# Kernel tuning notes

Hardware: AMD Instinct MI355X
Metric: run time of the kernel (lower is better)

## Reference

```python
import jax, jax.numpy as jnp
import numpy as np

NUM_NODES = 100000
NUM_EDGES = 1600000
DIM = 64
TAU = 0.5
EPS = 1e-12
SURGERY_EPS = 1e-6


def setup_inputs() -> dict:
    key = jax.random.key(0)
    k1, k2, k3, k4, k5 = jax.random.split(key, 5)
    x = jax.random.normal(k1, (NUM_NODES, DIM), dtype=jnp.float32)
    edge_index = jax.random.randint(k2, (2, NUM_EDGES), 0, NUM_NODES, dtype=jnp.int64)
    edge_weight = jax.random.uniform(k3, (NUM_EDGES,), dtype=jnp.float32)
    # nn.Linear weights (no bias): y = x @ W.T
    W_self = jax.random.normal(k4, (DIM, DIM), dtype=jnp.float32) / np.sqrt(DIM)
    W_neigh = jax.random.normal(k5, (DIM, DIM), dtype=jnp.float32) / np.sqrt(DIM)
    return {"x": x, "edge_index": edge_index, "edge_weight": edge_weight,
            "W_self": W_self, "W_neigh": W_neigh}


def reference(x, edge_index, edge_weight, W_self, W_neigh):
    num_nodes = x.shape[0]
    row, col = edge_index[0], edge_index[1]

    # --- Ollivier-Ricci (LLY limit-free combinatorial lower-bound) curvature per edge ---
    deg = jax.ops.segment_sum(edge_weight, row, num_segments=num_nodes)  # weighted out-degree
    inv_du = 1.0 / jnp.maximum(deg[row], EPS)
    inv_dv = 1.0 / jnp.maximum(deg[col], EPS)
    kappa = 2.0 * inv_du + 2.0 * inv_dv - 2.0  # [E]

    # --- CFL-stable step size for the Ricci flow ---
    delta_t = 0.5 / (jnp.max(jnp.abs(kappa)) + 1e-6)

    # --- Ricci-flow half step: dw/dt = -kappa * w ---
    w_half = jnp.maximum(edge_weight * (1.0 - 0.5 * delta_t * kappa), 0.0)

    # --- metric surgery: drop degenerate edges (implemented as a zero-weight mask,
    #     keeping edge count static so the kernel is jit-compatible) ---
    mask = w_half > SURGERY_EPS
    w_half = jnp.where(mask, w_half, 0.0)

    # --- row normalisation ---
    row_sum = jax.ops.segment_sum(w_half, row, num_segments=num_nodes)
    w_norm = w_half / jnp.maximum(row_sum[row], EPS)

    # --- Laplacian off-diagonals: L_uv = -w_norm  =>  -L_uv = w_norm ---
    minus_L = w_norm

    # --- incident mean curvature per node (over surviving edges) -> curvature gate ---
    cnt = jax.ops.segment_sum(mask.astype(x.dtype), row, num_segments=num_nodes)
    k_sum = jax.ops.segment_sum(jnp.where(mask, kappa, 0.0), row, num_segments=num_nodes)
    mean_kappa = k_sum / jnp.maximum(cnt, 1.0)
    rho = jax.nn.sigmoid(mean_kappa)  # [N]

    # --- gated message passing ---
    h_self = x @ W_self.T    # [N, D]
    h_neigh = x @ W_neigh.T  # [N, D]
    msg = minus_L[:, None] * h_neigh[col]                      # [E, D] gather + scale
    neigh_aggr = jax.ops.segment_sum(msg, row, num_segments=num_nodes)  # scatter-add

    # h0 buffer == first-forward x (detached)
    out = rho[:, None] * h_self + neigh_aggr + TAU * x
    return out, edge_index, w_norm
```

## Files before the change

### kernel.cpp

```cpp
#include <hip/hip_runtime.h>
#include <math.h>

#define NNODES 100000
#define NEDGES 1600000
#define DIM 64
#define TAU 0.5f
#define EPSF 1e-12f
#define SEPS 1e-6f

#define K 256
#define RPB 391
#define TILE 4096
#define EPT 8
#define CAP 7168
#define MAXK_GRID 512

typedef unsigned long long ull;
typedef unsigned short u16;
typedef __attribute__((ext_vector_type(8))) short bf16x8;
typedef __attribute__((ext_vector_type(4))) float f32x4;

__device__ __forceinline__ float bf2f(u16 h) {
    return __uint_as_float((unsigned)h << 16);
}
__device__ __forceinline__ u16 f2bf(float f) {
    unsigned u = __float_as_uint(f);
    u += 0x7FFFu + ((u >> 16) & 1);
    return (u16)(u >> 16);
}

__global__ __launch_bounds__(256) void k_init(int* __restrict__ bcur,
                                              float* __restrict__ maxabs) {
    bcur[threadIdx.x] = threadIdx.x * CAP;
    if (threadIdx.x < 4) maxabs[threadIdx.x] = 0.0f;
}

__global__ __launch_bounds__(512) void k_bin(const int* __restrict__ ei, const float* __restrict__ w,
                                             int* __restrict__ bcur, ull* __restrict__ arena,
                                             int E, int N) {
    __shared__ ull stg[TILE];
    __shared__ unsigned char bkt[TILE];
    __shared__ int cnt[K], lscan[K], gbase[K], cur[K], sc[K];
    __shared__ int tot;
    int t = threadIdx.x;
    int e0 = blockIdx.x * TILE;
    if (t < K) { cnt[t] = 0; cur[t] = 0; }
    __syncthreads();
    ull rec[EPT];
    int bb[EPT];
#pragma unroll
    for (int j = 0; j < EPT; j++) {
        int e = e0 + t + j * 512;
        bb[j] = -1;
        if (e < E) {
            int r = min(max(ei[e], 0), N - 1);
            int c = min(max(ei[E + e], 0), N - 1);
            float wv = w[e];
            int b = r / RPB, lr = r - b * RPB;
            rec[j] = ((ull)__float_as_uint(wv) << 32) | (unsigned)(c | (lr << 17));
            bb[j] = b;
            atomicAdd(&cnt[b], 1);
        }
    }
    __syncthreads();
    int v = (t < K) ? cnt[t] : 0;
    if (t < K) sc[t] = v;
    __syncthreads();
    for (int o = 1; o < K; o <<= 1) {
        int a = (t >= o && t < K) ? sc[t - o] : 0;
        __syncthreads();
        if (t < K) sc[t] += a;
        __syncthreads();
    }
    if (t < K) {
        lscan[t] = sc[t] - v;
        if (v > 0) gbase[t] = atomicAdd(&bcur[t], v);
        if (t == K - 1) tot = sc[t];
    }
    __syncthreads();
#pragma unroll
    for (int j = 0; j < EPT; j++) {
        if (bb[j] >= 0) {
            int p = lscan[bb[j]] + atomicAdd(&cur[bb[j]], 1);
            stg[p] = rec[j];
            bkt[p] = (unsigned char)bb[j];
        }
    }
    __syncthreads();
    int T = tot;
    for (int i = t; i < T; i += 512) {
        int b = bkt[i];
        size_t pos = (size_t)gbase[b] + (i - lscan[b]);
        if (pos < (size_t)(b + 1) * CAP) arena[pos] = stg[i];
    }
}

__global__ __launch_bounds__(512) void k_sort(const int* __restrict__ bcur,
                                              ull* __restrict__ arena,
                                              float* __restrict__ invdeg,
                                              int* __restrict__ off, int* __restrict__ degi,
                                              int N) {
    __shared__ ull stg[CAP];
    __shared__ int hist[RPB];
    __shared__ float degl[RPB];
    __shared__ int cur[RPB];
    __shared__ int sc[512];
    int t = threadIdx.x, b = blockIdx.x;
    int base = b * CAP;
    int cnt = min(bcur[b] - base, CAP);
    for (int i = t; i < RPB; i += 512) { hist[i] = 0; degl[i] = 0.0f; cur[i] = 0; }
    __syncthreads();
    for (int i = t; i < cnt; i += 512) {
        ull rec = arena[base + i];
        stg[i] = rec;
        int lr = (int)((rec >> 17) & 0x1FF);
        atomicAdd(&hist[lr], 1);
        atomicAdd(&degl[lr], __uint_as_float((unsigned)(rec >> 32)));
    }
    __syncthreads();
    int v = (t < RPB) ? hist[t] : 0;
    sc[t] = v;
    __syncthreads();
    for (int o = 1; o < 512; o <<= 1) {
        int a = (t >= o) ? sc[t - o] : 0;
        __syncthreads();
        sc[t] += a;
        __syncthreads();
    }
    int ex = sc[t] - v;
    if (t < RPB) {
        hist[t] = ex;
        int rn = b * RPB + t;
        if (rn < N) {
            off[rn] = base + ex; degi[rn] = v;
            invdeg[rn] = 1.0f / fmaxf(degl[t], EPSF);
        }
    }
    __syncthreads();
    int2* out2 = (int2*)arena;
    for (int i = t; i < cnt; i += 512) {
        ull rec = stg[i];
        int lr = (int)((rec >> 17) & 0x1FF);
        int p = hist[lr] + atomicAdd(&cur[lr], 1);
        out2[base + p] = make_int2((int)(rec & 0x1FFFF), (int)(unsigned)(rec >> 32));
    }
}

__global__ __launch_bounds__(256) void k_maxk(const int* __restrict__ ei,
                                              const float* __restrict__ invdeg,
                                              float* __restrict__ maxabs, int E, int N) {
    float m = 0.0f;
    int stride = gridDim.x * 256;
    for (int e = blockIdx.x * 256 + threadIdx.x; e < E; e += stride) {
        int r = min(max(ei[e], 0), N - 1);
        int c = min(max(ei[E + e], 0), N - 1);
        m = fmaxf(m, fabsf(2.0f * invdeg[r] + 2.0f * invdeg[c] - 2.0f));
    }
    for (int o = 32; o > 0; o >>= 1) m = fmaxf(m, __shfl_down(m, o, 64));
    __shared__ float red[4];
    int lane = threadIdx.x & 63, wid = threadIdx.x >> 6;
    if (lane == 0) red[wid] = m;
    __syncthreads();
    if (threadIdx.x == 0) {
        float bm = fmaxf(fmaxf(red[0], red[1]), fmaxf(red[2], red[3]));
        atomicMax((unsigned int*)maxabs, __float_as_uint(bm));
    }
}

#define WL(mp, d, kk) (((mp) * 64 + (d)) * 72 + (kk))
__global__ __launch_bounds__(256) void k_gemm(const float* __restrict__ x,
                                              const float* __restrict__ Wself,
                                              const float* __restrict__ Wneigh,
                                              u16* __restrict__ hneigh_h,
                                              float* __restrict__ out, int N) {
    __shared__ u16 wlds[4 * 64 * 72];
    int t = threadIdx.x;
    for (int i = t; i < 4096; i += 256) {
        int d = i >> 6, k = i & 63;
        float v = Wself[i];
        u16 h = f2bf(v);
        u16 lo = f2bf(v - bf2f(h));
        wlds[WL(0, d, k)] = h;
        wlds[WL(1, d, k)] = lo;
        v = Wneigh[i];
        h = f2bf(v);
        lo = f2bf(v - bf2f(h));
        wlds[WL(2, d, k)] = h;
        wlds[WL(3, d, k)] = lo;
    }
    __syncthreads();
    int w = t >> 6, l = t & 63;
    int m = l & 15, kg = l >> 4;
    int n0 = blockIdx.x * 64 + w * 16;
    if (n0 >= N) return;
    int nodeA = n0 + m;
    bf16x8 ah[2], al[2];
#pragma unroll
    for (int ks = 0; ks < 2; ks++) {
        float v[8];
        if (nodeA < N) {
            const float4* xp = (const float4*)(x + (size_t)nodeA * 64 + ks * 32 + kg * 8);
            float4 v0 = xp[0], v1 = xp[1];
            v[0] = v0.x; v[1] = v0.y; v[2] = v0.z; v[3] = v0.w;
            v[4] = v1.x; v[5] = v1.y; v[6] = v1.z; v[7] = v1.w;
        } else {
#pragma unroll
            for (int j = 0; j < 8; j++) v[j] = 0.0f;
        }
#pragma unroll
        for (int j = 0; j < 8; j++) {
            u16 h = f2bf(v[j]);
            u16 lo = f2bf(v[j] - bf2f(h));
            ah[ks][j] = (short)h;
            al[ks][j] = (short)lo;
        }
    }
    f32x4 accS[4], accN[4];
#pragma unroll
    for (int dt = 0; dt < 4; dt++) {
        accS[dt] = (f32x4){0.0f, 0.0f, 0.0f, 0.0f};
        accN[dt] = (f32x4){0.0f, 0.0f, 0.0f, 0.0f};
    }
#pragma unroll
    for (int dt = 0; dt < 4; dt++) {
        int d = dt * 16 + m;
#pragma unroll
        for (int ks = 0; ks < 2; ks++) {
            int kof = ks * 32 + kg * 8;
            bf16x8 bsh = *(const bf16x8*)&wlds[WL(0, d, kof)];
            bf16x8 bsl = *(const bf16x8*)&wlds[WL(1, d, kof)];
            bf16x8 bnh = *(const bf16x8*)&wlds[WL(2, d, kof)];
            bf16x8 bnl = *(const bf16x8*)&wlds[WL(3, d, kof)];
            accS[dt] = __builtin_amdgcn_mfma_f32_16x16x32_bf16(ah[ks], bsh, accS[dt], 0, 0, 0);
            accS[dt] = __builtin_amdgcn_mfma_f32_16x16x32_bf16(al[ks], bsh, accS[dt], 0, 0, 0);
            accS[dt] = __builtin_amdgcn_mfma_f32_16x16x32_bf16(ah[ks], bsl, accS[dt], 0, 0, 0);
            accN[dt] = __builtin_amdgcn_mfma_f32_16x16x32_bf16(ah[ks], bnh, accN[dt], 0, 0, 0);
            accN[dt] = __builtin_amdgcn_mfma_f32_16x16x32_bf16(al[ks], bnh, accN[dt], 0, 0, 0);
            accN[dt] = __builtin_amdgcn_mfma_f32_16x16x32_bf16(ah[ks], bnl, accN[dt], 0, 0, 0);
        }
    }
    int rbase = kg * 4;
#pragma unroll
    for (int r = 0; r < 4; r++) {
        int nn = n0 + rbase + r;
        if (nn >= N) continue;
#pragma unroll
        for (int dt = 0; dt < 4; dt++) {
            int d = dt * 16 + m;
            size_t idx = (size_t)nn * 64 + d;
            out[idx] = accS[dt][r];
            hneigh_h[idx] = f2bf(accN[dt][r]);
        }
    }
}

__global__ __launch_bounds__(256) void k_aggr(const int* __restrict__ off,
                                              const int* __restrict__ degi,
                                              const float* __restrict__ invdeg,
                                              const int2* __restrict__ csr,
                                              const float* __restrict__ maxabs,
                                              const float* __restrict__ x,
                                              const u16* __restrict__ hneigh_h,
                                              float* __restrict__ row_sum,
                                              float* __restrict__ out, int N) {
    int t = threadIdx.x;
    int lane = t & 63;
    int q = lane & 15;
    int g = lane >> 4;
    int n = blockIdx.x * 4 + (t >> 6);
    if (n >= N) return;
    int s = off[n], end = s + degi[n];
    float dt = 0.5f / (*maxabs + 1e-6f);
    float c1 = -0.5f * dt;
    float a = 2.0f * invdeg[n] - 2.0f;
    const ushort4* hn4 = (const ushort4*)hneigh_h;
    float a0 = 0.0f, a1 = 0.0f, a2 = 0.0f, a3 = 0.0f;
    float rs = 0.0f, ks = 0.0f, ct = 0.0f;
    int i = s;
    for (; i + 16 <= end; i += 16) {
        int2 p0 = csr[i + g];
        int2 p1 = csr[i + 4 + g];
        int2 p2 = csr[i + 8 + g];
        int2 p3 = csr[i + 12 + g];
        ushort4 h0 = hn4[(unsigned)((p0.x << 4) | q)];
        ushort4 h1 = hn4[(unsigned)((p1.x << 4) | q)];
        ushort4 h2 = hn4[(unsigned)((p2.x << 4) | q)];
        ushort4 h3 = hn4[(unsigned)((p3.x << 4) | q)];
        float k0 = fmaf(2.0f, invdeg[p0.x], a), k1 = fmaf(2.0f, invdeg[p1.x], a);
        float k2 = fmaf(2.0f, invdeg[p2.x], a), k3 = fmaf(2.0f, invdeg[p3.x], a);
        float w0 = __int_as_float(p0.y) * fmaf(c1, k0, 1.0f);
        float w1 = __int_as_float(p1.y) * fmaf(c1, k1, 1.0f);
        float w2 = __int_as_float(p2.y) * fmaf(c1, k2, 1.0f);
        float w3 = __int_as_float(p3.y) * fmaf(c1, k3, 1.0f);
        bool m0 = w0 > SEPS, m1 = w1 > SEPS, m2 = w2 > SEPS, m3 = w3 > SEPS;
        w0 = m0 ? w0 : 0.0f;
        w1 = m1 ? w1 : 0.0f;
        w2 = m2 ? w2 : 0.0f;
        w3 = m3 ? w3 : 0.0f;
        rs += (w0 + w1) + (w2 + w3);
        ks += ((m0 ? k0 : 0.0f) + (m1 ? k1 : 0.0f)) + ((m2 ? k2 : 0.0f) + (m3 ? k3 : 0.0f));
        ct += ((m0 ? 1.0f : 0.0f) + (m1 ? 1.0f : 0.0f)) + ((m2 ? 1.0f : 0.0f) + (m3 ? 1.0f : 0.0f));
        a0 = fmaf(w0, bf2f(h0.x), a0); a1 = fmaf(w0, bf2f(h0.y), a1);
        a2 = fmaf(w0, bf2f(h0.z), a2); a3 = fmaf(w0, bf2f(h0.w), a3);
        a0 = fmaf(w1, bf2f(h1.x), a0); a1 = fmaf(w1, bf2f(h1.y), a1);
        a2 = fmaf(w1, bf2f(h1.z), a2); a3 = fmaf(w1, bf2f(h1.w), a3);
        a0 = fmaf(w2, bf2f(h2.x), a0); a1 = fmaf(w2, bf2f(h2.y), a1);
        a2 = fmaf(w2, bf2f(h2.z), a2); a3 = fmaf(w2, bf2f(h2.w), a3);
        a0 = fmaf(w3, bf2f(h3.x), a0); a1 = fmaf(w3, bf2f(h3.y), a1);
        a2 = fmaf(w3, bf2f(h3.z), a2); a3 = fmaf(w3, bf2f(h3.w), a3);
    }
    for (; i < end; i += 4) {
        int e = i + g;
        bool v = e < end;
        int2 p = make_int2(0, 0);
        if (v) p = csr[e];
        ushort4 h = hn4[(unsigned)((p.x << 4) | q)];
        float kk = fmaf(2.0f, invdeg[p.x], a);
        float wv = __int_as_float(p.y) * fmaf(c1, kk, 1.0f);
        bool m = v && (wv > SEPS);
        wv = m ? wv : 0.0f;
        rs += wv;
        ks += m ? kk : 0.0f;
        ct += m ? 1.0f : 0.0f;
        a0 = fmaf(wv, bf2f(h.x), a0);
        a1 = fmaf(wv, bf2f(h.y), a1);
        a2 = fmaf(wv, bf2f(h.z), a2);
        a3 = fmaf(wv, bf2f(h.w), a3);
    }
    a0 += __shfl_xor(a0, 16, 64);
    a1 += __shfl_xor(a1, 16, 64);
    a2 += __shfl_xor(a2, 16, 64);
    a3 += __shfl_xor(a3, 16, 64);
    rs += __shfl_xor(rs, 16, 64);
    ks += __shfl_xor(ks, 16, 64);
    ct += __shfl_xor(ct, 16, 64);
    a0 += __shfl_xor(a0, 32, 64);
    a1 += __shfl_xor(a1, 32, 64);
    a2 += __shfl_xor(a2, 32, 64);
    a3 += __shfl_xor(a3, 32, 64);
    rs += __shfl_xor(rs, 32, 64);
    ks += __shfl_xor(ks, 32, 64);
    ct += __shfl_xor(ct, 32, 64);
    float mk = ks / fmaxf(ct, 1.0f);
    float rho = 1.0f / (1.0f + expf(-mk));
    float inv_rs = 1.0f / fmaxf(rs, EPSF);
    if (g == 0) {
        float4* o4 = (float4*)(out + (size_t)n * 64);
        const float4* x4 = (const float4*)(x + (size_t)n * 64);
        float4 o = o4[q];
        float4 xv = x4[q];
        o.x = fmaf(rho, o.x, fmaf(TAU, xv.x, a0 * inv_rs));
        o.y = fmaf(rho, o.y, fmaf(TAU, xv.y, a1 * inv_rs));
        o.z = fmaf(rho, o.z, fmaf(TAU, xv.z, a2 * inv_rs));
        o.w = fmaf(rho, o.w, fmaf(TAU, xv.w, a3 * inv_rs));
        o4[q] = o;
        if (q == 0) row_sum[n] = rs;
    }
}

__global__ void k_final(const int* __restrict__ ei, const float* __restrict__ w,
                        const float* __restrict__ invdeg, const float* __restrict__ row_sum,
                        const float* __restrict__ maxabs,
                        float* __restrict__ out_ei, float* __restrict__ out_wn, int E, int N) {
    int e = blockIdx.x * blockDim.x + threadIdx.x;
    if (e >= E) return;
    int r0 = ei[e], c0 = ei[E + e];
    int r = min(max(r0, 0), N - 1);
    int c = min(max(c0, 0), N - 1);
    float dt = 0.5f / (*maxabs + 1e-6f);
    float kap = 2.0f * invdeg[r] + 2.0f * invdeg[c] - 2.0f;
    float wh = fmaxf(w[e] * (1.0f - 0.5f * dt * kap), 0.0f);
    if (wh <= SEPS) wh = 0.0f;
    out_wn[e] = wh / fmaxf(row_sum[r], EPSF);
    out_ei[e] = (float)r0;
    out_ei[E + e] = (float)c0;
}

extern "C" void kernel_launch(void* const* d_in, const int* in_sizes, int n_in,
                              void* d_out, int out_size, void* d_ws, size_t ws_size,
                              hipStream_t stream) {
    (void)in_sizes; (void)n_in; (void)out_size; (void)ws_size;
    const int N = NNODES, E = NEDGES;

    const float* x      = (const float*)d_in[0];
    const int*   ei     = (const int*)d_in[1];
    const float* w      = (const float*)d_in[2];
    const float* Wself  = (const float*)d_in[3];
    const float* Wneigh = (const float*)d_in[4];

    float* out    = (float*)d_out;
    float* out_ei = out + (size_t)N * DIM;
    float* out_wn = out_ei + 2 * (size_t)E;

    ull*  arena = (ull*)out_ei;
    int2* csr   = (int2*)out_ei;

    float* invdeg  = (float*)d_ws;
    int*   off     = (int*)d_ws + (size_t)N;
    int*   degi    = (int*)d_ws + 2 * (size_t)N;
    float* row_sum = (float*)d_ws + 3 * (size_t)N;
    float* maxabs  = row_sum + (size_t)N;
    int*   bcur    = (int*)(maxabs + 4);
    u16*   hneigh_h = (u16*)((float*)d_ws + 4 * (size_t)N + 288);

    k_init<<<1, 256, 0, stream>>>(bcur, maxabs);
    k_bin<<<(E + TILE - 1) / TILE, 512, 0, stream>>>(ei, w, bcur, arena, E, N);
    k_sort<<<K, 512, 0, stream>>>(bcur, arena, invdeg, off, degi, N);
    k_maxk<<<MAXK_GRID, 256, 0, stream>>>(ei, invdeg, maxabs, E, N);
    k_gemm<<<(N + 63) / 64, 256, 0, stream>>>(x, Wself, Wneigh, hneigh_h, out, N);
    k_aggr<<<(N + 3) / 4, 256, 0, stream>>>(off, degi, invdeg, csr, maxabs, x,
                                            hneigh_h, row_sum, out, N);
    k_final<<<(E + 255) / 256, 256, 0, stream>>>(ei, w, invdeg, row_sum, maxabs,
                                                 out_ei, out_wn, E, N);
}
```

Baseline: 243.1 us.

## Fuse per-bucket sort and dense GEMM into one heterogeneous launch

```diff
diff --git a/kernel.cpp b/kernel.cpp
--- a/kernel.cpp
+++ b/kernel.cpp
@@ -14,6 +14,7 @@
 #define EPT 8
 #define CAP 7168
 #define MAXK_GRID 512
+#define GEMM_BLKS ((NNODES + 127) / 128)
 
 typedef unsigned long long ull;
 typedef unsigned short u16;
@@ -95,54 +96,149 @@
     }
 }
 
-__global__ __launch_bounds__(512) void k_sort(const int* __restrict__ bcur,
-                                              ull* __restrict__ arena,
-                                              float* __restrict__ invdeg,
-                                              int* __restrict__ off, int* __restrict__ degi,
-                                              int N) {
-    __shared__ ull stg[CAP];
-    __shared__ int hist[RPB];
-    __shared__ float degl[RPB];
-    __shared__ int cur[RPB];
-    __shared__ int sc[512];
-    int t = threadIdx.x, b = blockIdx.x;
-    int base = b * CAP;
-    int cnt = min(bcur[b] - base, CAP);
-    for (int i = t; i < RPB; i += 512) { hist[i] = 0; degl[i] = 0.0f; cur[i] = 0; }
-    __syncthreads();
-    for (int i = t; i < cnt; i += 512) {
-        ull rec = arena[base + i];
-        stg[i] = rec;
-        int lr = (int)((rec >> 17) & 0x1FF);
-        atomicAdd(&hist[lr], 1);
-        atomicAdd(&degl[lr], __uint_as_float((unsigned)(rec >> 32)));
-    }
-    __syncthreads();
-    int v = (t < RPB) ? hist[t] : 0;
-    sc[t] = v;
-    __syncthreads();
-    for (int o = 1; o < 512; o <<= 1) {
-        int a = (t >= o) ? sc[t - o] : 0;
-        __syncthreads();
-        sc[t] += a;
-        __syncthreads();
-    }
-    int ex = sc[t] - v;
-    if (t < RPB) {
-        hist[t] = ex;
-        int rn = b * RPB + t;
-        if (rn < N) {
-            off[rn] = base + ex; degi[rn] = v;
-            invdeg[rn] = 1.0f / fmaxf(degl[t], EPSF);
-        }
-    }
-    __syncthreads();
-    int2* out2 = (int2*)arena;
-    for (int i = t; i < cnt; i += 512) {
-        ull rec = stg[i];
-        int lr = (int)((rec >> 17) & 0x1FF);
-        int p = hist[lr] + atomicAdd(&cur[lr], 1);
-        out2[base + p] = make_int2((int)(rec & 0x1FFFF), (int)(unsigned)(rec >> 32));
+struct SortSmem {
+    ull stg[CAP];
+    int hist[RPB];
+    float degl[RPB];
+    int cur[RPB];
+    int sc[512];
+};
+struct GemmSmem {
+    u16 wlds[4 * 64 * 72];
+};
+#define WL(mp, d, kk) (((mp) * 64 + (d)) * 72 + (kk))
+
+__global__ __launch_bounds__(512) void k_sg(const int* __restrict__ bcur,
+                                            ull* __restrict__ arena,
+                                            float* __restrict__ invdeg,
+                                            int* __restrict__ off, int* __restrict__ degi,
+                                            const float* __restrict__ x,
+                                            const float* __restrict__ Wself,
+                                            const float* __restrict__ Wneigh,
+                                            u16* __restrict__ hneigh_h,
+                                            float* __restrict__ out, int N) {
+    __shared__ __align__(16) char smraw[sizeof(SortSmem)];
+    int t = threadIdx.x;
+    if (blockIdx.x < K) {
+        SortSmem* sm = (SortSmem*)smraw;
+        int b = blockIdx.x;
+        int base = b * CAP;
+        int cnt = min(bcur[b] - base, CAP);
+        for (int i = t; i < RPB; i += 512) { sm->hist[i] = 0; sm->degl[i] = 0.0f; sm->cur[i] = 0; }
+        __syncthreads();
+        for (int i = t; i < cnt; i += 512) {
+            ull rec = arena[base + i];
+            sm->stg[i] = rec;
+            int lr = (int)((rec >> 17) & 0x1FF);
+            atomicAdd(&sm->hist[lr], 1);
+            atomicAdd(&sm->degl[lr], __uint_as_float((unsigned)(rec >> 32)));
+        }
+        __syncthreads();
+        int v = (t < RPB) ? sm->hist[t] : 0;
+        sm->sc[t] = v;
+        __syncthreads();
+        for (int o = 1; o < 512; o <<= 1) {
+            int a = (t >= o) ? sm->sc[t - o] : 0;
+            __syncthreads();
+            sm->sc[t] += a;
+            __syncthreads();
+        }
+        int ex = sm->sc[t] - v;
+        if (t < RPB) {
+            sm->hist[t] = ex;
+            int rn = b * RPB + t;
+            if (rn < N) {
+                off[rn] = base + ex; degi[rn] = v;
+                invdeg[rn] = 1.0f / fmaxf(sm->degl[t], EPSF);
+            }
+        }
+        __syncthreads();
+        int2* out2 = (int2*)arena;
+        for (int i = t; i < cnt; i += 512) {
+            ull rec = sm->stg[i];
+            int lr = (int)((rec >> 17) & 0x1FF);
+            int p = sm->hist[lr] + atomicAdd(&sm->cur[lr], 1);
+            out2[base + p] = make_int2((int)(rec & 0x1FFFF), (int)(unsigned)(rec >> 32));
+        }
+    } else {
+        GemmSmem* sm = (GemmSmem*)smraw;
+        for (int i = t; i < 4096; i += 512) {
+            int d = i >> 6, k = i & 63;
+            float v = Wself[i];
+            u16 h = f2bf(v);
+            u16 lo = f2bf(v - bf2f(h));
+            sm->wlds[WL(0, d, k)] = h;
+            sm->wlds[WL(1, d, k)] = lo;
+            v = Wneigh[i];
+            h = f2bf(v);
+            lo = f2bf(v - bf2f(h));
+            sm->wlds[WL(2, d, k)] = h;
+            sm->wlds[WL(3, d, k)] = lo;
+        }
+        __syncthreads();
+        int w = t >> 6, l = t & 63;
+        int m = l & 15, kg = l >> 4;
+        int n0 = (blockIdx.x - K) * 128 + w * 16;
+        if (n0 >= N) return;
+        int nodeA = n0 + m;
+        bf16x8 ah[2], al[2];
+#pragma unroll
+        for (int ks = 0; ks < 2; ks++) {
+            float v[8];
+            if (nodeA < N) {
+                const float4* xp = (const float4*)(x + (size_t)nodeA * 64 + ks * 32 + kg * 8);
+                float4 v0 = xp[0], v1 = xp[1];
+                v[0] = v0.x; v[1] = v0.y; v[2] = v0.z; v[3] = v0.w;
+                v[4] = v1.x; v[5] = v1.y; v[6] = v1.z; v[7] = v1.w;
+            } else {
+#pragma unroll
+                for (int j = 0; j < 8; j++) v[j] = 0.0f;
+            }
+#pragma unroll
+            for (int j = 0; j < 8; j++) {
+                u16 h = f2bf(v[j]);
+                u16 lo = f2bf(v[j] - bf2f(h));
+                ah[ks][j] = (short)h;
+                al[ks][j] = (short)lo;
+            }
+        }
+        f32x4 accS[4], accN[4];
+#pragma unroll
+        for (int dt = 0; dt < 4; dt++) {
+            accS[dt] = (f32x4){0.0f, 0.0f, 0.0f, 0.0f};
+            accN[dt] = (f32x4){0.0f, 0.0f, 0.0f, 0.0f};
+        }
+#pragma unroll
+        for (int dt = 0; dt < 4; dt++) {
+            int d = dt * 16 + m;
+#pragma unroll
+            for (int ks = 0; ks < 2; ks++) {
+                int kof = ks * 32 + kg * 8;
+                bf16x8 bsh = *(const bf16x8*)&sm->wlds[WL(0, d, kof)];
+                bf16x8 bsl = *(const bf16x8*)&sm->wlds[WL(1, d, kof)];
+                bf16x8 bnh = *(const bf16x8*)&sm->wlds[WL(2, d, kof)];
+                bf16x8 bnl = *(const bf16x8*)&sm->wlds[WL(3, d, kof)];
+                accS[dt] = __builtin_amdgcn_mfma_f32_16x16x32_bf16(ah[ks], bsh, accS[dt], 0, 0, 0);
+                accS[dt] = __builtin_amdgcn_mfma_f32_16x16x32_bf16(al[ks], bsh, accS[dt], 0, 0, 0);
+                accS[dt] = __builtin_amdgcn_mfma_f32_16x16x32_bf16(ah[ks], bsl, accS[dt], 0, 0, 0);
+                accN[dt] = __builtin_amdgcn_mfma_f32_16x16x32_bf16(ah[ks], bnh, accN[dt], 0, 0, 0);
+                accN[dt] = __builtin_amdgcn_mfma_f32_16x16x32_bf16(al[ks], bnh, accN[dt], 0, 0, 0);
+                accN[dt] = __builtin_amdgcn_mfma_f32_16x16x32_bf16(ah[ks], bnl, accN[dt], 0, 0, 0);
+            }
+        }
+        int rbase = kg * 4;
+#pragma unroll
+        for (int r = 0; r < 4; r++) {
+            int nn = n0 + rbase + r;
+            if (nn >= N) continue;
+#pragma unroll
+            for (int dt = 0; dt < 4; dt++) {
+                int d = dt * 16 + m;
+                size_t idx = (size_t)nn * 64 + d;
+                out[idx] = accS[dt][r];
+                hneigh_h[idx] = f2bf(accN[dt][r]);
+            }
+        }
     }
 }
 
@@ -164,93 +260,6 @@
     if (threadIdx.x == 0) {
         float bm = fmaxf(fmaxf(red[0], red[1]), fmaxf(red[2], red[3]));
         atomicMax((unsigned int*)maxabs, __float_as_uint(bm));
-    }
-}
-
-#define WL(mp, d, kk) (((mp) * 64 + (d)) * 72 + (kk))
-__global__ __launch_bounds__(256) void k_gemm(const float* __restrict__ x,
-                                              const float* __restrict__ Wself,
-                                              const float* __restrict__ Wneigh,
-                                              u16* __restrict__ hneigh_h,
-                                              float* __restrict__ out, int N) {
-    __shared__ u16 wlds[4 * 64 * 72];
-    int t = threadIdx.x;
-    for (int i = t; i < 4096; i += 256) {
-        int d = i >> 6, k = i & 63;
-        float v = Wself[i];
-        u16 h = f2bf(v);
-        u16 lo = f2bf(v - bf2f(h));
-        wlds[WL(0, d, k)] = h;
-        wlds[WL(1, d, k)] = lo;
-        v = Wneigh[i];
-        h = f2bf(v);
-        lo = f2bf(v - bf2f(h));
-        wlds[WL(2, d, k)] = h;
-        wlds[WL(3, d, k)] = lo;
-    }
-    __syncthreads();
-    int w = t >> 6, l = t & 63;
-    int m = l & 15, kg = l >> 4;
-    int n0 = blockIdx.x * 64 + w * 16;
-    if (n0 >= N) return;
-    int nodeA = n0 + m;
-    bf16x8 ah[2], al[2];
-#pragma unroll
-    for (int ks = 0; ks < 2; ks++) {
-        float v[8];
-        if (nodeA < N) {
-            const float4* xp = (const float4*)(x + (size_t)nodeA * 64 + ks * 32 + kg * 8);
-            float4 v0 = xp[0], v1 = xp[1];
-            v[0] = v0.x; v[1] = v0.y; v[2] = v0.z; v[3] = v0.w;
-            v[4] = v1.x; v[5] = v1.y; v[6] = v1.z; v[7] = v1.w;
-        } else {
-#pragma unroll
-            for (int j = 0; j < 8; j++) v[j] = 0.0f;
-        }
-#pragma unroll
-        for (int j = 0; j < 8; j++) {
-            u16 h = f2bf(v[j]);
-            u16 lo = f2bf(v[j] - bf2f(h));
-            ah[ks][j] = (short)h;
-            al[ks][j] = (short)lo;
-        }
-    }
-    f32x4 accS[4], accN[4];
-#pragma unroll
-    for (int dt = 0; dt < 4; dt++) {
-        accS[dt] = (f32x4){0.0f, 0.0f, 0.0f, 0.0f};
-        accN[dt] = (f32x4){0.0f, 0.0f, 0.0f, 0.0f};
-    }
-#pragma unroll
-    for (int dt = 0; dt < 4; dt++) {
-        int d = dt * 16 + m;
-#pragma unroll
-        for (int ks = 0; ks < 2; ks++) {
-            int kof = ks * 32 + kg * 8;
-            bf16x8 bsh = *(const bf16x8*)&wlds[WL(0, d, kof)];
-            bf16x8 bsl = *(const bf16x8*)&wlds[WL(1, d, kof)];
-            bf16x8 bnh = *(const bf16x8*)&wlds[WL(2, d, kof)];
-            bf16x8 bnl = *(const bf16x8*)&wlds[WL(3, d, kof)];
-            accS[dt] = __builtin_amdgcn_mfma_f32_16x16x32_bf16(ah[ks], bsh, accS[dt], 0, 0, 0);
-            accS[dt] = __builtin_amdgcn_mfma_f32_16x16x32_bf16(al[ks], bsh, accS[dt], 0, 0, 0);
-            accS[dt] = __builtin_amdgcn_mfma_f32_16x16x32_bf16(ah[ks], bsl, accS[dt], 0, 0, 0);
-            accN[dt] = __builtin_amdgcn_mfma_f32_16x16x32_bf16(ah[ks], bnh, accN[dt], 0, 0, 0);
-            accN[dt] = __builtin_amdgcn_mfma_f32_16x16x32_bf16(al[ks], bnh, accN[dt], 0, 0, 0);
-            accN[dt] = __builtin_amdgcn_mfma_f32_16x16x32_bf16(ah[ks], bnl, accN[dt], 0, 0, 0);
-        }
-    }
-    int rbase = kg * 4;
-#pragma unroll
-    for (int r = 0; r < 4; r++) {
-        int nn = n0 + rbase + r;
-        if (nn >= N) continue;
-#pragma unroll
-        for (int dt = 0; dt < 4; dt++) {
-            int d = dt * 16 + m;
-            size_t idx = (size_t)nn * 64 + d;
-            out[idx] = accS[dt][r];
-            hneigh_h[idx] = f2bf(accN[dt][r]);
-        }
     }
 }
 
@@ -405,9 +414,9 @@
 
     k_init<<<1, 256, 0, stream>>>(bcur, maxabs);
     k_bin<<<(E + TILE - 1) / TILE, 512, 0, stream>>>(ei, w, bcur, arena, E, N);
-    k_sort<<<K, 512, 0, stream>>>(bcur, arena, invdeg, off, degi, N);
+    k_sg<<<K + GEMM_BLKS, 512, 0, stream>>>(bcur, arena, invdeg, off, degi,
+                                            x, Wself, Wneigh, hneigh_h, out, N);
     k_maxk<<<MAXK_GRID, 256, 0, stream>>>(ei, invdeg, maxabs, E, N);
-    k_gemm<<<(N + 63) / 64, 256, 0, stream>>>(x, Wself, Wneigh, hneigh_h, out, N);
     k_aggr<<<(N + 3) / 4, 256, 0, stream>>>(off, degi, invdeg, csr, maxabs, x,
                                             hneigh_h, row_sum, out, N);
     k_final<<<(E + 255) / 256, 256, 0, stream>>>(ei, w, invdeg, row_sum, maxabs,
```

After: 238.5 us. About the same (-1.9%).
